# Performance work log

Measured on AMD Instinct MI355X. Metric: run time of the kernel, lower is better.

## Reference

```python
import jax, jax.numpy as jnp
import numpy as np

B, S, DIM = 1, 2048, 1024
HEADS, KV_HEADS, DH = 16, 2, 64
GQ = HEADS // KV_HEADS
CBS = 64   # compress block size
SBS = 64   # selection block size
NUM_SEL = 8
WIN = 512  # sliding window size
NUM_MEM = 1
SCALE = DH ** -0.5
NEG = -jnp.finfo(jnp.float32).max


def setup_inputs():
    ks = jax.random.split(jax.random.key(0), 12)
    cdim = CBS * DH
    dim_inner = HEADS * DH
    dim_kv = KV_HEADS * DH
    p = lambda k, shape: jax.random.normal(k, shape, jnp.float32) * 0.02
    return {
        "x": jax.random.normal(ks[0], (B, S, DIM), jnp.float32),
        "rms_g": jnp.ones((DIM,), jnp.float32),
        "W_qkv": p(ks[1], (DIM, dim_inner + 2 * dim_kv)),
        "k_pos": p(ks[2], (KV_HEADS, CBS, DH)),
        "v_pos": p(ks[3], (KV_HEADS, CBS, DH)),
        "mem_kv": p(ks[4], (2, KV_HEADS, NUM_MEM, DH)),
        "kW1": p(ks[5], (cdim, cdim)), "kb1": jnp.zeros((cdim,), jnp.float32),
        "kW2": p(ks[6], (cdim, DH)), "kb2": jnp.zeros((DH,), jnp.float32),
        "vW1": p(ks[7], (cdim, cdim)), "vb1": jnp.zeros((cdim,), jnp.float32),
        "vW2": p(ks[8], (cdim, DH)), "vb2": jnp.zeros((DH,), jnp.float32),
        "W_comb": p(ks[9], (DIM, 3 * HEADS)),
        "b_comb": jnp.tile(jnp.array([-2.0, -2.0, 2.0], jnp.float32), HEADS),
        "W_out": p(ks[10], (HEADS * DH, DIM)),
    }


def _rot_half(u):
    v = u.reshape(u.shape[:-1] + (DH // 2, 2))
    return jnp.stack([-v[..., 1], v[..., 0]], axis=-1).reshape(u.shape)


def reference(x, rms_g, W_qkv, k_pos, v_pos, mem_kv, kW1, kb1, kW2, kb2,
              vW1, vb1, vW2, vb2, W_comb, b_comb, W_out):
    n_cb = S // CBS
    n_fb = S // SBS
    num_sel = min(NUM_SEL, n_cb)

    # RMSNorm
    xn = x * jax.lax.rsqrt(jnp.mean(x * x, -1, keepdims=True) + jnp.finfo(jnp.float32).eps) * rms_g

    qkv = xn @ W_qkv
    q, k, v = jnp.split(qkv, [HEADS * DH, (HEADS + KV_HEADS) * DH], axis=-1)
    q = q.reshape(B, S, HEADS, DH).transpose(0, 2, 1, 3)       # b h n d
    k = k.reshape(B, S, KV_HEADS, DH).transpose(0, 2, 1, 3)
    v = v.reshape(B, S, KV_HEADS, DH).transpose(0, 2, 1, 3)

    # ---- compressed branch: per-block MLP compression of K/V ----
    kc = (k + jnp.tile(k_pos, (1, n_cb, 1))[None]).reshape(B, KV_HEADS, n_cb, CBS * DH)
    vc = (v + jnp.tile(v_pos, (1, n_cb, 1))[None]).reshape(B, KV_HEADS, n_cb, CBS * DH)
    ck = jax.nn.relu(kc @ kW1 + kb1) @ kW2 + kb2               # b h w d
    cv = jax.nn.relu(vc @ vW1 + vb1) @ vW2 + vb2
    ck = jnp.concatenate([jnp.broadcast_to(mem_kv[0], (B, KV_HEADS, NUM_MEM, DH)), ck], axis=2)
    cv = jnp.concatenate([jnp.broadcast_to(mem_kv[1], (B, KV_HEADS, NUM_MEM, DH)), cv], axis=2)
    ck_seq = jnp.concatenate([jnp.full((NUM_MEM,), -1), (jnp.arange(n_cb) + 1) * CBS - 1])
    cmask = ck_seq[None, :] < jnp.arange(S)[:, None]           # [S, mem+n_cb]
    qg = q.reshape(B, KV_HEADS, GQ, S, DH)
    csim = jnp.einsum('bhgid,bhjd->bhgij', qg, ck) * SCALE
    csim = jnp.where(cmask, csim, NEG)
    c_out = jnp.einsum('bhgij,bhjd->bhgid', jax.nn.softmax(csim, -1), cv).reshape(B, HEADS, S, DH)

    # ---- rotary embedding (interleaved pairs, theta=10000) ----
    inv_freq = 1.0 / (10000.0 ** (jnp.arange(0, DH, 2, dtype=jnp.float32) / DH))
    freqs = jnp.repeat(jnp.arange(S, dtype=jnp.float32)[:, None] * inv_freq, 2, axis=-1)
    cos, sin = jnp.cos(freqs), jnp.sin(freqs)
    rq = q * cos + _rot_half(q) * sin
    rk = k * cos + _rot_half(k) * sin

    # ---- block selection from compressed attention scores ----
    imp = csim[..., NUM_MEM:].mean(axis=2)                     # mean over grouped queries: [B,KVH,S,n_cb]
    imp = jnp.concatenate([jnp.full(imp.shape[:-1] + (1,), -1000.0), imp], -1)
    imp = jax.nn.softmax(imp, -1)[..., 1:]
    sel_val, sel_idx = jax.lax.top_k(imp, num_sel)             # [B,KVH,S,sel]
    fmask = jnp.broadcast_to((sel_val > 1e-10)[..., None], (B, KV_HEADS, S, num_sel, SBS))
    diag_idx = jnp.broadcast_to((jnp.arange(S) // SBS)[None, None, :, None], (B, KV_HEADS, S, 1))
    sel_idx = jnp.concatenate([sel_idx, diag_idx], -1)         # append own (diagonal) block
    causal = jnp.tril(jnp.ones((SBS, SBS), bool))
    diag_mask = jnp.broadcast_to(jnp.tile(causal, (n_fb, 1))[None, None, :, None, :], (B, KV_HEADS, S, 1, SBS))
    fmask = jnp.concatenate([fmask, diag_mask], axis=-2).reshape(B, KV_HEADS, S, (num_sel + 1) * SBS)

    # ---- fine attention over gathered selected blocks ----
    fkb = rk.reshape(B, KV_HEADS, 1, n_fb, SBS, DH)
    fvb = v.reshape(B, KV_HEADS, 1, n_fb, SBS, DH)
    gi = sel_idx[..., None, None]                              # [B,KVH,S,sel+1,1,1]
    fk = jnp.take_along_axis(fkb, gi, axis=3).reshape(B, KV_HEADS, S, (num_sel + 1) * SBS, DH)
    fv = jnp.take_along_axis(fvb, gi, axis=3).reshape(B, KV_HEADS, S, (num_sel + 1) * SBS, DH)
    fqg = rq.reshape(B, KV_HEADS, GQ, S, DH)
    fsim = jnp.einsum('bhgid,bhijd->bhgij', fqg, fk) * SCALE
    fsim = jnp.where(fmask[:, :, None], fsim, NEG)
    f_out = jnp.einsum('bhgij,bhijd->bhgid', jax.nn.softmax(fsim, -1), fv).reshape(B, HEADS, S, DH)

    # ---- causal sliding window (exact window, look_backward=1) ----
    skf = jnp.repeat(rk, GQ, axis=1)
    svf = jnp.repeat(v, GQ, axis=1)
    nw = S // WIN
    kw = skf.reshape(B, HEADS, nw, WIN, DH)
    vw = svf.reshape(B, HEADS, nw, WIN, DH)
    kcat = jnp.concatenate([jnp.pad(kw, ((0, 0), (0, 0), (1, 0), (0, 0), (0, 0)))[:, :, :nw], kw], axis=3)
    vcat = jnp.concatenate([jnp.pad(vw, ((0, 0), (0, 0), (1, 0), (0, 0), (0, 0)))[:, :, :nw], vw], axis=3)
    qw = rq.reshape(B, HEADS, nw, WIN, DH)
    gq_pos = jnp.arange(nw)[:, None, None] * WIN + jnp.arange(WIN)[None, :, None]
    gk_pos = jnp.arange(nw)[:, None, None] * WIN - WIN + jnp.arange(2 * WIN)[None, None, :]
    smask = (gk_pos >= 0) & (gk_pos <= gq_pos) & (gq_pos - gk_pos <= WIN)
    ssim = jnp.where(smask, jnp.einsum('bhwid,bhwjd->bhwij', qw, kcat) * SCALE, NEG)
    s_out = jnp.einsum('bhwij,bhwjd->bhwid', jax.nn.softmax(ssim, -1), vcat).reshape(B, HEADS, S, DH)

    # ---- learned per-token, per-head strategy combination ----
    gates = jax.nn.sigmoid(xn @ W_comb + b_comb).reshape(B, S, HEADS, 3).transpose(0, 2, 1, 3)
    out = gates[..., 0:1] * c_out + gates[..., 1:2] * f_out + gates[..., 2:3] * s_out
    return out.transpose(0, 2, 1, 3).reshape(B, S, HEADS * DH) @ W_out
```

## Files before the change

kernel.cpp:

```cpp
#include <hip/hip_runtime.h>
#include <hip/hip_bf16.h>
#include <cstddef>
#include <cstdint>

#define S      2048
#define DIM    1024
#define HEADS  16
#define KVH    2
#define GQ     8
#define DH     64
#define CBS    64
#define SBS    64
#define NUMSEL 8
#define WIN    512
#define NCB    (S / CBS)
#define CDIM   (CBS * DH)
#define QKVC   (HEADS * DH + 2 * KVH * DH)
#define KOFF   (HEADS * DH)
#define VOFF   (HEADS * DH + KVH * DH)
#define SCALE  0.125f
#define RMS_EPS 1.1920928955078125e-07f

typedef __attribute__((ext_vector_type(8))) short bf16x8;
typedef __attribute__((ext_vector_type(4))) float f32x4;

__device__ inline short f2bs(float f) {
    __hip_bfloat16 b = __float2bfloat16(f);
    return *(short*)&b;
}

__device__ inline float wave_sum(float v) {
    for (int o = 32; o > 0; o >>= 1) v += __shfl_xor(v, o);
    return v;
}

__global__ __launch_bounds__(256) void rmsnorm_kernel(
        const float* __restrict__ x, const float* __restrict__ g,
        float* __restrict__ xn, __hip_bfloat16* __restrict__ xnb) {
    int s = blockIdx.x, tid = threadIdx.x;
    const float4* row = (const float4*)(x + (size_t)s * DIM);
    float4 v = row[tid];
    float ss = v.x * v.x + v.y * v.y + v.z * v.z + v.w * v.w;
    ss = wave_sum(ss);
    __shared__ float red[4];
    if ((tid & 63) == 0) red[tid >> 6] = ss;
    __syncthreads();
    float tot = red[0] + red[1] + red[2] + red[3];
    float sc = rsqrtf(tot / (float)DIM + RMS_EPS);
    float4 gg = ((const float4*)g)[tid];
    float4 o;
    o.x = v.x * sc * gg.x; o.y = v.y * sc * gg.y;
    o.z = v.z * sc * gg.z; o.w = v.w * sc * gg.w;
    ((float4*)(xn + (size_t)s * DIM))[tid] = o;
    size_t b = (size_t)s * DIM + tid * 4;
    xnb[b + 0] = __float2bfloat16(o.x);
    xnb[b + 1] = __float2bfloat16(o.y);
    xnb[b + 2] = __float2bfloat16(o.z);
    xnb[b + 3] = __float2bfloat16(o.w);
}

__global__ __launch_bounds__(256) void cast_bf16_kernel(
        const float* __restrict__ in, __hip_bfloat16* __restrict__ out, int n4) {
    int e = blockIdx.x * 256 + threadIdx.x;
    if (e >= n4) return;
    float4 v = ((const float4*)in)[e];
    out[4 * e + 0] = __float2bfloat16(v.x);
    out[4 * e + 1] = __float2bfloat16(v.y);
    out[4 * e + 2] = __float2bfloat16(v.z);
    out[4 * e + 3] = __float2bfloat16(v.w);
}

__global__ __launch_bounds__(256) void transpose_cast_kernel(
        const float* __restrict__ W, short* __restrict__ Wt, int K, int N) {
    __shared__ float tile[64][65];
    int n0 = blockIdx.x * 64, k0 = blockIdx.y * 64;
    int tid = threadIdx.x;
    #pragma unroll
    for (int e = 0; e < 16; e++) {
        int idx = tid + e * 256;
        int r = idx >> 6, c = idx & 63;
        float v = 0.f;
        if (n0 + c < N) v = W[(size_t)(k0 + r) * N + n0 + c];
        tile[r][c] = v;
    }
    __syncthreads();
    #pragma unroll
    for (int e = 0; e < 16; e++) {
        int idx = tid + e * 256;
        int r = idx >> 6, c = idx & 63;
        if (n0 + r < N)
            Wt[(size_t)(n0 + r) * K + k0 + c] = f2bs(tile[c][r]);
    }
}

__global__ __launch_bounds__(256) void cast_v_kernel(
        const float* __restrict__ qkv, short* __restrict__ vb) {
    int e = blockIdx.x * 256 + threadIdx.x;
    if (e >= S * KVH * DH / 4) return;
    int idx = e * 4;
    int tok = idx / (KVH * DH), rem = idx % (KVH * DH);
    float4 v = *(const float4*)(qkv + (size_t)tok * QKVC + VOFF + rem);
    vb[idx + 0] = f2bs(v.x);
    vb[idx + 1] = f2bs(v.y);
    vb[idx + 2] = f2bs(v.z);
    vb[idx + 3] = f2bs(v.w);
}

template <int BM, int BN, int WM, int WN, int ACT>
__global__ __launch_bounds__(256) void gemm_bt_kernel(
        const __hip_bfloat16* __restrict__ A, const short* __restrict__ Bt,
        const float* __restrict__ bias, float* __restrict__ C,
        int M, int N, int K) {
    constexpr int BK = 32;
    constexpr int TM = BM / (WM * 16);
    constexpr int TN = BN / (WN * 16);
    constexpr int LDK = BK + 8;
    __shared__ short As[BM][LDK];
    __shared__ short Bs[BN][LDK];
    int tid = threadIdx.x;
    int wave = tid >> 6, lane = tid & 63;
    int wm = wave % WM, wn = wave / WM;
    int m0 = wm * TM * 16, n0 = wn * TN * 16;
    int bm = blockIdx.y * BM, bn = blockIdx.x * BN;
    int lm = lane & 15, quad = lane >> 4;
    const short* Ash = (const short*)A;
    f32x4 acc[TM][TN] = {};
    for (int k0 = 0; k0 < K; k0 += BK) {
        #pragma unroll
        for (int e = 0; e < BM * BK / (256 * 8); e++) {
            int idx = (tid + e * 256) * 8;
            int r = idx >> 5, kk = idx & 31;
            *(bf16x8*)(&As[r][kk]) =
                *(const bf16x8*)(Ash + (size_t)(bm + r) * K + k0 + kk);
        }
        #pragma unroll
        for (int e = 0; e < BN * BK / (256 * 8); e++) {
            int idx = (tid + e * 256) * 8;
            int r = idx >> 5, kk = idx & 31;
            bf16x8 v = {};
            if (bn + r < N)
                v = *(const bf16x8*)(Bt + (size_t)(bn + r) * K + k0 + kk);
            *(bf16x8*)(&Bs[r][kk]) = v;
        }
        __syncthreads();
        bf16x8 af[TM], bf_[TN];
        #pragma unroll
        for (int i = 0; i < TM; i++)
            af[i] = *(const bf16x8*)(&As[m0 + i * 16 + lm][quad * 8]);
        #pragma unroll
        for (int j = 0; j < TN; j++)
            bf_[j] = *(const bf16x8*)(&Bs[n0 + j * 16 + lm][quad * 8]);
        #pragma unroll
        for (int i = 0; i < TM; i++)
            #pragma unroll
            for (int j = 0; j < TN; j++)
                acc[i][j] = __builtin_amdgcn_mfma_f32_16x16x32_bf16(
                    af[i], bf_[j], acc[i][j], 0, 0, 0);
        __syncthreads();
    }
    #pragma unroll
    for (int i = 0; i < TM; i++) {
        #pragma unroll
        for (int j = 0; j < TN; j++) {
            int gn = bn + n0 + j * 16 + lm;
            if (gn >= N) continue;
            #pragma unroll
            for (int r = 0; r < 4; r++) {
                int gm = bm + m0 + i * 16 + quad * 4 + r;
                float v = acc[i][j][r];
                if (bias) v += bias[gn];
                if (ACT == 2) v = 1.f / (1.f + expf(-v));
                C[(size_t)gm * N + gn] = v;
            }
        }
    }
}

template <int BM, int BN, int WM, int WN>
__global__ __launch_bounds__(256) void gemm_mfma_kernel(
        const __hip_bfloat16* __restrict__ A, const float* __restrict__ B,
        float* __restrict__ C, int M, int N, int K, int kslice) {
    constexpr int BK = 32;
    constexpr int TM = BM / (WM * 16);
    constexpr int TN = BN / (WN * 16);
    constexpr int LDK = BK + 8;
    constexpr int NB = BN * BK / 256;
    __shared__ __hip_bfloat16 As[BM][LDK];
    __shared__ __hip_bfloat16 Bs[BN][LDK];
    int tid = threadIdx.x;
    int wave = tid >> 6, lane = tid & 63;
    int wm = wave % WM, wn = wave / WM;
    int m0 = wm * TM * 16, n0 = wn * TN * 16;
    int bm = blockIdx.y * BM, bn = blockIdx.x * BN;
    int kbeg = blockIdx.z * kslice, kend = kbeg + kslice;
    int lm = lane & 15, quad = lane >> 4;
    f32x4 acc[TM][TN] = {};
    for (int k0 = kbeg; k0 < kend; k0 += BK) {
        #pragma unroll
        for (int e = 0; e < BM * BK / (256 * 8); e++) {
            int idx = (tid + e * 256) * 8;
            int r = idx >> 5, kk = idx & 31;
            *(bf16x8*)(&As[r][kk]) =
                *(const bf16x8*)(A + (size_t)(bm + r) * K + k0 + kk);
        }
        float tmpB[NB];
        #pragma unroll
        for (int e = 0; e < NB; e++) {
            int idx = tid + e * 256;
            int kk = idx / BN, n = idx % BN;
            tmpB[e] = B[(size_t)(k0 + kk) * N + bn + n];
        }
        #pragma unroll
        for (int e = 0; e < NB; e++) {
            int idx = tid + e * 256;
            int kk = idx / BN, n = idx % BN;
            Bs[n][kk] = __float2bfloat16(tmpB[e]);
        }
        __syncthreads();
        bf16x8 af[TM], bf_[TN];
        #pragma unroll
        for (int i = 0; i < TM; i++)
            af[i] = *(const bf16x8*)(&As[m0 + i * 16 + lm][quad * 8]);
        #pragma unroll
        for (int j = 0; j < TN; j++)
            bf_[j] = *(const bf16x8*)(&Bs[n0 + j * 16 + lm][quad * 8]);
        #pragma unroll
        for (int i = 0; i < TM; i++)
            #pragma unroll
            for (int j = 0; j < TN; j++)
                acc[i][j] = __builtin_amdgcn_mfma_f32_16x16x32_bf16(
                    af[i], bf_[j], acc[i][j], 0, 0, 0);
        __syncthreads();
    }
    size_t cbase = (size_t)blockIdx.z * M * N;
    #pragma unroll
    for (int i = 0; i < TM; i++) {
        #pragma unroll
        for (int j = 0; j < TN; j++) {
            int gn = bn + n0 + j * 16 + lm;
            #pragma unroll
            for (int r = 0; r < 4; r++) {
                int gm = bm + m0 + i * 16 + quad * 4 + r;
                C[cbase + (size_t)gm * N + gn] = acc[i][j][r];
            }
        }
    }
}

__global__ __launch_bounds__(256) void gemm_splitk_kernel(
        const float* __restrict__ A, const float* __restrict__ B,
        float* __restrict__ P, int M, int N, int K, int kslice) {
    const int BM = 64, BN = 64, BK = 16;
    __shared__ float As[BK][BM + 4];
    __shared__ float Bs[BK][BN];
    int bm = blockIdx.y * BM, bn = blockIdx.x * BN;
    int z = blockIdx.z;
    int kbeg = z * kslice, kend = kbeg + kslice;
    int tid = threadIdx.x;
// ... 129 lines not shown
    }
    for (int e = t; e < NCB * DH; e += 64) {
        int w = e >> 6, d = e & 63;
        ckl[w * 65 + d] = ck[((size_t)kvh * (NCB + 1) + 1 + w) * DH + d];
    }
    __syncthreads();
    if (t < NCB) {
        int w = t;
        float val;
        if (w * CBS + CBS - 1 < s) {
            float acc = 0.f;
            #pragma unroll
            for (int g = 0; g < GQ; g++) {
                const float* qp = qg + g * DH;
                const float* cp = ckl + w * 65;
                #pragma unroll 16
                for (int d = 0; d < DH; d++) acc += qp[d] * cp[d];
            }
            val = acc * SCALE * (1.f / (float)GQ);
        } else {
            val = -INFINITY;
        }
        imp[((size_t)kvh * S + s) * NCB + w] = val;
    }
}

__global__ __launch_bounds__(256) void select_kernel(
        const float* __restrict__ imp, int* __restrict__ sel) {
    int idx = blockIdx.x * 256 + threadIdx.x;
    if (idx >= KVH * S) return;
    const float* row = imp + (size_t)idx * NCB;
    float p[NCB];
    float m = -1000.f;
    for (int w = 0; w < NCB; w++) { p[w] = row[w]; m = fmaxf(m, p[w]); }
    float z = expf(-1000.f - m);
    for (int w = 0; w < NCB; w++) { p[w] = expf(p[w] - m); z += p[w]; }
    float inv = 1.f / z;
    bool used[NCB];
    for (int w = 0; w < NCB; w++) used[w] = false;
    for (int i = 0; i < NUMSEL; i++) {
        int best = 0; float bv = -1.f;
        for (int w = 0; w < NCB; w++) {
            if (!used[w]) {
                float pw = p[w] * inv;
                if (pw > bv) { bv = pw; best = w; }
            }
        }
        used[best] = true;
        sel[(size_t)idx * NUMSEL + i] = (bv > 1e-10f) ? best : -1;
    }
}

__global__ __launch_bounds__(256) void cattn_kernel(
        const float* __restrict__ qkv, const short* __restrict__ ck16,
        const short* __restrict__ cv16, const float* __restrict__ gates,
        float* __restrict__ attn) {
    int h = blockIdx.x, qb = blockIdx.y;
    int kvh = h >> 3;
    int tid = threadIdx.x;
    int wv = tid >> 6, lane = tid & 63;
    int lm = lane & 15, quad = lane >> 4;
    __shared__ short Qb[64][72];
    __shared__ short Ks[64][72];
    __shared__ short Vt[64][72];
    __shared__ short Pb[64][72];
    for (int e = tid; e < 1024; e += 256) {
        int q = e >> 4, d4 = (e & 15) * 4;
        float4 v = *(const float4*)(qkv + (size_t)(qb * 64 + q) * QKVC + h * DH + d4);
        Qb[q][d4 + 0] = f2bs(v.x); Qb[q][d4 + 1] = f2bs(v.y);
        Qb[q][d4 + 2] = f2bs(v.z); Qb[q][d4 + 3] = f2bs(v.w);
    }
    for (int e = tid; e < 512; e += 256) {
        int c8 = e >> 6, j = e & 63;
        bf16x8 kv = {}, vv = {};
        if (j < NCB + 1) {
            kv = *(const bf16x8*)(ck16 + ((size_t)kvh * (NCB + 1) + j) * DH + c8 * 8);
            vv = *(const bf16x8*)(cv16 + ((size_t)kvh * (NCB + 1) + j) * DH + c8 * 8);
        }
        #pragma unroll
        for (int t = 0; t < 8; t++) {
            Ks[j][c8 * 8 + t] = kv[t];
            Vt[c8 * 8 + t][j] = vv[t];
        }
    }
    __syncthreads();
    bf16x8 aq0 = *(const bf16x8*)&Qb[wv * 16 + lm][quad * 8];
    bf16x8 aq1 = *(const bf16x8*)&Qb[wv * 16 + lm][32 + quad * 8];
    int vismax = (qb < NCB) ? qb : NCB;
    f32x4 sc[4];
    #pragma unroll
    for (int t = 0; t < 4; t++) {
        bf16x8 bk0 = *(const bf16x8*)&Ks[t * 16 + lm][quad * 8];
        bf16x8 bk1 = *(const bf16x8*)&Ks[t * 16 + lm][32 + quad * 8];
        f32x4 s4 = {0.f, 0.f, 0.f, 0.f};
        s4 = __builtin_amdgcn_mfma_f32_16x16x32_bf16(aq0, bk0, s4, 0, 0, 0);
        s4 = __builtin_amdgcn_mfma_f32_16x16x32_bf16(aq1, bk1, s4, 0, 0, 0);
        sc[t] = s4;
    }
    float l[4];
    float pr[4][4];
    #pragma unroll
    for (int r = 0; r < 4; r++) {
        float mx = -INFINITY;
        #pragma unroll
        for (int t = 0; t < 4; t++) {
            int jj = t * 16 + lm;
            bool vis = (jj == 0) || (jj <= vismax);
            float v = vis ? sc[t][r] * SCALE : -INFINITY;
            sc[t][r] = v;
            mx = fmaxf(mx, v);
        }
        #pragma unroll
        for (int o = 1; o < 16; o <<= 1) mx = fmaxf(mx, __shfl_xor(mx, o));
        float sum = 0.f;
        #pragma unroll
        for (int t = 0; t < 4; t++) {
            float p = __expf(sc[t][r] - mx);
            pr[r][t] = p;
            sum += p;
        }
        #pragma unroll
        for (int o = 1; o < 16; o <<= 1) sum += __shfl_xor(sum, o);
        l[r] = sum;
    }
    #pragma unroll
    for (int r = 0; r < 4; r++)
        #pragma unroll
        for (int t = 0; t < 4; t++)
            Pb[wv * 16 + quad * 4 + r][t * 16 + lm] = f2bs(pr[r][t]);
    __syncthreads();
    bf16x8 ap0 = *(const bf16x8*)&Pb[wv * 16 + lm][quad * 8];
    bf16x8 ap1 = *(const bf16x8*)&Pb[wv * 16 + lm][32 + quad * 8];
    f32x4 oacc[4];
    #pragma unroll
    for (int t = 0; t < 4; t++) {
        bf16x8 bv0 = *(const bf16x8*)&Vt[t * 16 + lm][quad * 8];
        bf16x8 bv1 = *(const bf16x8*)&Vt[t * 16 + lm][32 + quad * 8];
        f32x4 a = {0.f, 0.f, 0.f, 0.f};
        a = __builtin_amdgcn_mfma_f32_16x16x32_bf16(ap0, bv0, a, 0, 0, 0);
        a = __builtin_amdgcn_mfma_f32_16x16x32_bf16(ap1, bv1, a, 0, 0, 0);
        oacc[t] = a;
    }
    #pragma unroll
    for (int r = 0; r < 4; r++) {
        int spos = qb * 64 + wv * 16 + quad * 4 + r;
        float g0 = gates[((size_t)spos * HEADS + h) * 3 + 0];
        float f = g0 / l[r];
        #pragma unroll
        for (int t = 0; t < 4; t++)
            attn[(size_t)spos * (HEADS * DH) + h * DH + t * 16 + lm] = oacc[t][r] * f;
    }
}

__global__ __launch_bounds__(64, 2) void fattn_kernel(
        const short* __restrict__ rqb, const short* __restrict__ rkb,
        const short* __restrict__ vb, const int* __restrict__ sel,
        const float* __restrict__ gates, float* __restrict__ attn) {
    int kvh = blockIdx.x, s = blockIdx.y;
    int lane = threadIdx.x;
    int lm = lane & 15, quad = lane >> 4;
    __shared__ short Vt[64][68];
    __shared__ short Pb[16][68];
    const short* qp = rqb + (size_t)s * (HEADS * DH) + (size_t)(kvh * 8 + (lm & 7)) * DH;
    bf16x8 aq0 = *(const bf16x8*)(qp + quad * 8);
    bf16x8 aq1 = *(const bf16x8*)(qp + 32 + quad * 8);
    int bl[9];
    {
        const int4* sp = (const int4*)(sel + ((size_t)kvh * S + s) * NUMSEL);
        int4 s0 = sp[0], s1 = sp[1];
        bl[0] = s0.x; bl[1] = s0.y; bl[2] = s0.z; bl[3] = s0.w;
        bl[4] = s1.x; bl[5] = s1.y; bl[6] = s1.z; bl[7] = s1.w;
        bl[8] = s >> 6;
    }
    float m[4], l[4];
    f32x4 oacc[4];
    #pragma unroll
    for (int r = 0; r < 4; r++) {
        m[r] = -INFINITY; l[r] = 0.f;
        oacc[r] = (f32x4){0.f, 0.f, 0.f, 0.f};
    }
    bf16x8 kpre[2][4][2];
    bf16x8 vpre[2][8];
    {
        int w0 = bl[0] < 0 ? 0 : bl[0];
        #pragma unroll
        for (int t = 0; t < 4; t++) {
            const short* kp = rkb + ((size_t)(w0 * SBS + t * 16 + lm) * KVH + kvh) * DH;
            kpre[0][t][0] = *(const bf16x8*)(kp + quad * 8);
            kpre[0][t][1] = *(const bf16x8*)(kp + 32 + quad * 8);
        }
        const short* vp = vb + ((size_t)(w0 * SBS + lane) * KVH + kvh) * DH;
        #pragma unroll
        for (int r = 0; r < 8; r++) vpre[0][r] = *(const bf16x8*)(vp + r * 8);
    }
    #pragma unroll
    for (int i = 0; i < 9; i++) {
        const int p = i & 1;
        const int pn = p ^ 1;
        if (i < 8) {
            int wn = bl[i + 1] < 0 ? 0 : bl[i + 1];
            #pragma unroll
            for (int t = 0; t < 4; t++) {
                const short* kp = rkb + ((size_t)(wn * SBS + t * 16 + lm) * KVH + kvh) * DH;
                kpre[pn][t][0] = *(const bf16x8*)(kp + quad * 8);
                kpre[pn][t][1] = *(const bf16x8*)(kp + 32 + quad * 8);
            }
            const short* vp = vb + ((size_t)(wn * SBS + lane) * KVH + kvh) * DH;
            #pragma unroll
            for (int r = 0; r < 8; r++) vpre[pn][r] = *(const bf16x8*)(vp + r * 8);
        }
        if (i < 8 && bl[i] < 0) continue;
        #pragma unroll
        for (int r = 0; r < 8; r++)
            #pragma unroll
            for (int t = 0; t < 8; t++) Vt[r * 8 + t][lane] = vpre[p][r][t];
        f32x4 sc[4];
        #pragma unroll
        for (int t = 0; t < 4; t++) {
            f32x4 s4 = {0.f, 0.f, 0.f, 0.f};
            s4 = __builtin_amdgcn_mfma_f32_16x16x32_bf16(aq0, kpre[p][t][0], s4, 0, 0, 0);
            s4 = __builtin_amdgcn_mfma_f32_16x16x32_bf16(aq1, kpre[p][t][1], s4, 0, 0, 0);
            sc[t] = s4;
        }
        bool diag = (i == 8);
        #pragma unroll
        for (int r = 0; r < 4; r++) {
            float mx = -INFINITY;
            #pragma unroll
            for (int t = 0; t < 4; t++) {
                int jj = t * 16 + lm;
                bool vis = !diag || (jj <= (s & 63));
                float v = vis ? sc[t][r] * SCALE : -INFINITY;
                sc[t][r] = v;
                mx = fmaxf(mx, v);
            }
            #pragma unroll
            for (int o = 1; o < 16; o <<= 1) mx = fmaxf(mx, __shfl_xor(mx, o));
            float mn = fmaxf(m[r], mx);
            float al = __expf(m[r] - mn);
            float sum = 0.f;
            #pragma unroll
            for (int t = 0; t < 4; t++) {
                float pv_ = __expf(sc[t][r] - mn);
                sc[t][r] = pv_;
                sum += pv_;
            }
            #pragma unroll
            for (int o = 1; o < 16; o <<= 1) sum += __shfl_xor(sum, o);
            l[r] = l[r] * al + sum;
            m[r] = mn;
            #pragma unroll
            for (int t = 0; t < 4; t++) oacc[t][r] *= al;
        }
        #pragma unroll
        for (int r = 0; r < 4; r++)
            #pragma unroll
            for (int t = 0; t < 4; t++)
                Pb[quad * 4 + r][t * 16 + lm] = f2bs(sc[t][r]);
        asm volatile("s_waitcnt lgkmcnt(0)" ::: "memory");
        bf16x8 ap0 = *(const bf16x8*)&Pb[lm][quad * 8];
        bf16x8 ap1 = *(const bf16x8*)&Pb[lm][32 + quad * 8];
        #pragma unroll
        for (int t = 0; t < 4; t++) {
            bf16x8 bv0 = *(const bf16x8*)&Vt[t * 16 + lm][quad * 8];
            bf16x8 bv1 = *(const bf16x8*)&Vt[t * 16 + lm][32 + quad * 8];
            oacc[t] = __builtin_amdgcn_mfma_f32_16x16x32_bf16(ap0, bv0, oacc[t], 0, 0, 0);
            oacc[t] = __builtin_amdgcn_mfma_f32_16x16x32_bf16(ap1, bv1, oacc[t], 0, 0, 0);
        }
    }
    if (quad < 2) {
        #pragma unroll
        for (int r = 0; r < 4; r++) {
            int head = kvh * 8 + quad * 4 + r;
            float fac = gates[((size_t)s * HEADS + head) * 3 + 1] / l[r];
            #pragma unroll
            for (int t = 0; t < 4; t++)
                attn[(size_t)s * (HEADS * DH) + head * DH + t * 16 + lm]
                    += oacc[t][r] * fac;
        }
    }
}

__global__ __launch_bounds__(256) void sattn_kernel(
        const short* __restrict__ rqb, const short* __restrict__ rkb,
        const short* __restrict__ vb, const float* __restrict__ gates,
        float* __restrict__ attn) {
    int h = blockIdx.x, qb = blockIdx.y;
    int kvh = h >> 3;
    int tid = threadIdx.x;
    int wv = tid >> 6, lane = tid & 63;
    int lm = lane & 15, quad = lane >> 4;
    __shared__ short Vt[2][64][72];
    __shared__ short Pb[64][72];
    const short* qp = rqb + (size_t)(qb * 64 + wv * 16 + lm) * (HEADS * DH) + h * DH;
    bf16x8 aq0 = *(const bf16x8*)(qp + quad * 8);
    bf16x8 aq1 = *(const bf16x8*)(qp + 32 + quad * 8);
    int myrow = wv * 16 + quad * 4;
    int j0 = tid & 63, c80 = tid >> 6;
    float m[4], l[4];
    f32x4 oacc[4];
    #pragma unroll
    for (int r = 0; r < 4; r++) { m[r] = -INFINITY; l[r] = 0.f; }
    #pragma unroll
    for (int t = 0; t < 4; t++) oacc[t] = (f32x4){0.f, 0.f, 0.f, 0.f};
    int nc = 0;
    for (int c = 0; c < 9; c++) {
        int kb = qb * 64 - WIN + c * 64;
        if (kb < 0) continue;
        const short* vp = vb + ((size_t)(kb + j0) * KVH + kvh) * DH;
        bf16x8 vv0 = *(const bf16x8*)(vp + c80 * 8);
        bf16x8 vv1 = *(const bf16x8*)(vp + (c80 + 4) * 8);
        f32x4 sc[4];
        #pragma unroll
        for (int t = 0; t < 4; t++) {
            const short* kp = rkb + ((size_t)(kb + t * 16 + lm) * KVH + kvh) * DH;
            bf16x8 bk0 = *(const bf16x8*)(kp + quad * 8);
            bf16x8 bk1 = *(const bf16x8*)(kp + 32 + quad * 8);
            f32x4 s4 = {0.f, 0.f, 0.f, 0.f};
            s4 = __builtin_amdgcn_mfma_f32_16x16x32_bf16(aq0, bk0, s4, 0, 0, 0);
            s4 = __builtin_amdgcn_mfma_f32_16x16x32_bf16(aq1, bk1, s4, 0, 0, 0);
            sc[t] = s4;
        }
        short* vtb = &Vt[nc & 1][0][0];
        #pragma unroll
        for (int t = 0; t < 8; t++) vtb[(size_t)(c80 * 8 + t) * 72 + j0] = vv0[t];
        #pragma unroll
        for (int t = 0; t < 8; t++) vtb[(size_t)((c80 + 4) * 8 + t) * 72 + j0] = vv1[t];
        __syncthreads();
        #pragma unroll
        for (int r = 0; r < 4; r++) {
            int row = myrow + r;
            float mx = -INFINITY;
            #pragma unroll
            for (int t = 0; t < 4; t++) {
                int jj = t * 16 + lm;
                bool vis = true;
                if (c == 0) vis = (jj >= row);
                if (c == 8) vis = (jj <= row);
                float v = vis ? sc[t][r] * SCALE : -INFINITY;
                sc[t][r] = v;
                mx = fmaxf(mx, v);
            }
            #pragma unroll
            for (int o = 1; o < 16; o <<= 1) mx = fmaxf(mx, __shfl_xor(mx, o));
            float mn = fmaxf(m[r], mx);
            float al = __expf(m[r] - mn);
            float sum = 0.f;
            #pragma unroll
            for (int t = 0; t < 4; t++) {
                float pv_ = __expf(sc[t][r] - mn);
                sc[t][r] = pv_;
                sum += pv_;
            }
            #pragma unroll
            for (int o = 1; o < 16; o <<= 1) sum += __shfl_xor(sum, o);
            l[r] = l[r] * al + sum;
            m[r] = mn;
            #pragma unroll
            for (int t = 0; t < 4; t++) oacc[t][r] *= al;
        }
        #pragma unroll
        for (int r = 0; r < 4; r++)
            #pragma unroll
            for (int t = 0; t < 4; t++)
                Pb[myrow + r][t * 16 + lm] = f2bs(sc[t][r]);
        asm volatile("s_waitcnt lgkmcnt(0)" ::: "memory");
        bf16x8 ap0 = *(const bf16x8*)&Pb[wv * 16 + lm][quad * 8];
        bf16x8 ap1 = *(const bf16x8*)&Pb[wv * 16 + lm][32 + quad * 8];
        #pragma unroll
        for (int t = 0; t < 4; t++) {
            bf16x8 bv0 = *(const bf16x8*)(vtb + (size_t)(t * 16 + lm) * 72 + quad * 8);
            bf16x8 bv1 = *(const bf16x8*)(vtb + (size_t)(t * 16 + lm) * 72 + 32 + quad * 8);
            oacc[t] = __builtin_amdgcn_mfma_f32_16x16x32_bf16(ap0, bv0, oacc[t], 0, 0, 0);
            oacc[t] = __builtin_amdgcn_mfma_f32_16x16x32_bf16(ap1, bv1, oacc[t], 0, 0, 0);
        }
        nc++;
    }
    #pragma unroll
    for (int r = 0; r < 4; r++) {
        int spos = qb * 64 + myrow + r;
        float g2 = gates[((size_t)spos * HEADS + h) * 3 + 2];
        float f = g2 / l[r];
        #pragma unroll
        for (int t = 0; t < 4; t++)
            attn[(size_t)spos * (HEADS * DH) + h * DH + t * 16 + lm] += oacc[t][r] * f;
    }
}

extern "C" void kernel_launch(void* const* d_in, const int* in_sizes, int n_in,
                              void* d_out, int out_size, void* d_ws, size_t ws_size,
                              hipStream_t stream) {
    const float* x      = (const float*)d_in[0];
    const float* rms_g  = (const float*)d_in[1];
    const float* W_qkv  = (const float*)d_in[2];
    const float* k_pos  = (const float*)d_in[3];
    const float* v_pos  = (const float*)d_in[4];
    const float* mem_kv = (const float*)d_in[5];
    const float* kW1    = (const float*)d_in[6];
    const float* kb1    = (const float*)d_in[7];
    const float* kW2    = (const float*)d_in[8];
    const float* kb2    = (const float*)d_in[9];
    const float* vW1    = (const float*)d_in[10];
    const float* vb1    = (const float*)d_in[11];
    const float* vW2    = (const float*)d_in[12];
    const float* vb2    = (const float*)d_in[13];
    const float* W_comb = (const float*)d_in[14];
    const float* b_comb = (const float*)d_in[15];
    const float* W_out  = (const float*)d_in[16];
    float* out = (float*)d_out;

    float* ws    = (float*)d_ws;
    float* xn    = ws;
    float* qkv   = xn    + (size_t)S * DIM;
    short* rqb   = (short*)(qkv + (size_t)S * QKVC);
    short* rkb   = (short*)((float*)rqb + 1048576);
    float* R     = (float*)rkb + 131072;
    float* ck    = R     + 1048576;
    float* cv    = ck    + (size_t)KVH * (NCB + 1) * DH;
    short* ck16  = (short*)(cv + (size_t)KVH * (NCB + 1) * DH);
    short* cv16  = (short*)((float*)ck16 + 2112);
    float* imp   = (float*)cv16 + 2112;
    float* gates = imp   + (size_t)KVH * S * NCB;
    float* attn  = gates + (size_t)S * HEADS * 3;
    int*   sel   = (int*)(attn + (size_t)S * HEADS * DH);
    float* WT    = attn + (size_t)S * HEADS * DH + 8192;
    short* wqkvT = (short*)WT;
    short* woutT = (short*)(WT + 655360);
    short* wcombT= (short*)(WT + 655360 + 524288);

    __hip_bfloat16* xnb   = (__hip_bfloat16*)R;
    __hip_bfloat16* kcmb  = (__hip_bfloat16*)R;
    __hip_bfloat16* vcmb  = (__hip_bfloat16*)(R + 131072);
    float* khid  = R + 262144;
    float* vhid  = R + 524288;
    float* ckb   = R + 786432;
    float* cvb   = R + 790528;
    __hip_bfloat16* attnb = (__hip_bfloat16*)R;
    short* vbb   = (short*)imp;
    float* partW1 = attn;
    float* partW2 = imp;

    transpose_cast_kernel<<<dim3(QKVC / 64, DIM / 64), 256, 0, stream>>>(W_qkv, wqkvT, DIM, QKVC);
    transpose_cast_kernel<<<dim3(DIM / 64, DIM / 64), 256, 0, stream>>>(W_out, woutT, DIM, DIM);
    transpose_cast_kernel<<<dim3(1, DIM / 64), 256, 0, stream>>>(W_comb, wcombT, DIM, HEADS * 3);
    rmsnorm_kernel<<<S, 256, 0, stream>>>(x, rms_g, xn, xnb);
    gemm_bt_kernel<64, 64, 2, 2, 0><<<dim3(QKVC / 64, S / 64), 256, 0, stream>>>(
        xnb, wqkvT, nullptr, qkv, S, QKVC, DIM);
    gemm_bt_kernel<64, 64, 2, 2, 2><<<dim3(1, S / 64), 256, 0, stream>>>(
        xnb, wcombT, b_comb, gates, S, HEADS * 3, DIM);
    rotary_kernel<<<S, 256, 0, stream>>>(qkv, rqb, rkb);
    build_cmat_kernel<<<KVH * NCB, 256, 0, stream>>>(qkv, k_pos, v_pos, kcmb, vcmb);
    gemm_mfma_kernel<64, 128, 1, 4><<<dim3(CDIM / 128, 1, 8), 256, 0, stream>>>(
        kcmb, kW1, partW1, 64, CDIM, CDIM, CDIM / 8);
    reduce_splitk_kernel<1><<<(64 * CDIM + 255) / 256, 256, 0, stream>>>(
        partW1, kb1, khid, 64 * CDIM, CDIM, 8);
    gemm_splitk_kernel<<<dim3(1, 1, 32), 256, 0, stream>>>(khid, kW2, partW2, 64, DH, CDIM, CDIM / 32);
    reduce_splitk_kernel<0><<<(64 * DH + 255) / 256, 256, 0, stream>>>(partW2, kb2, ckb, 64 * DH, DH, 32);
    gemm_mfma_kernel<64, 128, 1, 4><<<dim3(CDIM / 128, 1, 8), 256, 0, stream>>>(
        vcmb, vW1, partW1, 64, CDIM, CDIM, CDIM / 8);
    reduce_splitk_kernel<1><<<(64 * CDIM + 255) / 256, 256, 0, stream>>>(
        partW1, vb1, vhid, 64 * CDIM, CDIM, 8);
    gemm_splitk_kernel<<<dim3(1, 1, 32), 256, 0, stream>>>(vhid, vW2, partW2, 64, DH, CDIM, CDIM / 32);
    reduce_splitk_kernel<0><<<(64 * DH + 255) / 256, 256, 0, stream>>>(partW2, vb2, cvb, 64 * DH, DH, 32);
    assemble_kernel<<<(KVH * (NCB + 1) * DH + 255) / 256, 256, 0, stream>>>(
        ckb, cvb, mem_kv, ck, cv, ck16, cv16);
    imp_kernel<<<dim3(KVH, S), 64, 0, stream>>>(qkv, ck, imp);
    select_kernel<<<(KVH * S + 255) / 256, 256, 0, stream>>>(imp, sel);
    cast_v_kernel<<<(S * KVH * DH / 4 + 255) / 256, 256, 0, stream>>>(qkv, vbb);
    cattn_kernel<<<dim3(HEADS, S / 64), 256, 0, stream>>>(qkv, ck16, cv16, gates, attn);
    fattn_kernel<<<dim3(KVH, S), 64, 0, stream>>>(rqb, rkb, vbb, sel, gates, attn);
    sattn_kernel<<<dim3(HEADS, S / 64), 256, 0, stream>>>(rqb, rkb, vbb, gates, attn);
    cast_bf16_kernel<<<(S * HEADS * DH / 4 + 255) / 256, 256, 0, stream>>>(
        attn, attnb, S * HEADS * DH / 4);
    gemm_bt_kernel<64, 64, 2, 2, 0><<<dim3(DIM / 64, S / 64), 256, 0, stream>>>(
        attnb, woutT, nullptr, out, S, DIM, DIM);
}
```

Measured before the change: 559.9 us.

## Split fine-attention selected blocks across two wavefronts with LSE merge

The fine (selected-block) attention kernel now launches two wavefronts per block. One wavefront handles selected blocks 0-3 and the other handles blocks 4-7 plus the diagonal block, each keeping its own online-softmax state. The partial results are then merged through shared memory using the max and sum statistics. This is meant to halve the serial per-block latency and raise parallelism. In exchange it drops the register double-buffered prefetch of K/V, uses more shared memory, and adds two barriers.

```diff
diff --git a/kernel.cpp b/kernel.cpp
--- a/kernel.cpp
+++ b/kernel.cpp
@@ -539,15 +539,16 @@
     }
 }
 
-__global__ __launch_bounds__(64, 2) void fattn_kernel(
+__global__ __launch_bounds__(128) void fattn_kernel(
         const short* __restrict__ rqb, const short* __restrict__ rkb,
         const short* __restrict__ vb, const int* __restrict__ sel,
         const float* __restrict__ gates, float* __restrict__ attn) {
     int kvh = blockIdx.x, s = blockIdx.y;
-    int lane = threadIdx.x;
+    int tid = threadIdx.x;
+    int wv = tid >> 6, lane = tid & 63;
     int lm = lane & 15, quad = lane >> 4;
-    __shared__ short Vt[64][68];
-    __shared__ short Pb[16][68];
+    __shared__ short Vt[2][64][68];
+    __shared__ short Pb[2][16][68];
     const short* qp = rqb + (size_t)s * (HEADS * DH) + (size_t)(kvh * 8 + (lm & 7)) * DH;
     bf16x8 aq0 = *(const bf16x8*)(qp + quad * 8);
     bf16x8 aq1 = *(const bf16x8*)(qp + 32 + quad * 8);
@@ -566,49 +567,30 @@
         m[r] = -INFINITY; l[r] = 0.f;
         oacc[r] = (f32x4){0.f, 0.f, 0.f, 0.f};
     }
-    bf16x8 kpre[2][4][2];
-    bf16x8 vpre[2][8];
-    {
-        int w0 = bl[0] < 0 ? 0 : bl[0];
+    int ibeg = wv ? 4 : 0;
+    int iend = wv ? 9 : 4;
+    for (int i = ibeg; i < iend; i++) {
+        int w = bl[i];
+        if (i < NUMSEL && w < 0) continue;
+        const short* vp = vb + ((size_t)(w * SBS + lane) * KVH + kvh) * DH;
+        bf16x8 vv[8];
+        #pragma unroll
+        for (int r = 0; r < 8; r++) vv[r] = *(const bf16x8*)(vp + r * 8);
+        f32x4 sc[4];
         #pragma unroll
         for (int t = 0; t < 4; t++) {
-            const short* kp = rkb + ((size_t)(w0 * SBS + t * 16 + lm) * KVH + kvh) * DH;
-            kpre[0][t][0] = *(const bf16x8*)(kp + quad * 8);
-            kpre[0][t][1] = *(const bf16x8*)(kp + 32 + quad * 8);
-        }
-        const short* vp = vb + ((size_t)(w0 * SBS + lane) * KVH + kvh) * DH;
-        #pragma unroll
-        for (int r = 0; r < 8; r++) vpre[0][r] = *(const bf16x8*)(vp + r * 8);
-    }
-    #pragma unroll
-    for (int i = 0; i < 9; i++) {
-        const int p = i & 1;
-        const int pn = p ^ 1;
-        if (i < 8) {
-            int wn = bl[i + 1] < 0 ? 0 : bl[i + 1];
-            #pragma unroll
-            for (int t = 0; t < 4; t++) {
-                const short* kp = rkb + ((size_t)(wn * SBS + t * 16 + lm) * KVH + kvh) * DH;
-                kpre[pn][t][0] = *(const bf16x8*)(kp + quad * 8);
-                kpre[pn][t][1] = *(const bf16x8*)(kp + 32 + quad * 8);
-            }
-            const short* vp = vb + ((size_t)(wn * SBS + lane) * KVH + kvh) * DH;
-            #pragma unroll
-            for (int r = 0; r < 8; r++) vpre[pn][r] = *(const bf16x8*)(vp + r * 8);
-        }
-        if (i < 8 && bl[i] < 0) continue;
+            const short* kp = rkb + ((size_t)(w * SBS + t * 16 + lm) * KVH + kvh) * DH;
+            bf16x8 bk0 = *(const bf16x8*)(kp + quad * 8);
+            bf16x8 bk1 = *(const bf16x8*)(kp + 32 + quad * 8);
+            f32x4 s4 = {0.f, 0.f, 0.f, 0.f};
+            s4 = __builtin_amdgcn_mfma_f32_16x16x32_bf16(aq0, bk0, s4, 0, 0, 0);
+            s4 = __builtin_amdgcn_mfma_f32_16x16x32_bf16(aq1, bk1, s4, 0, 0, 0);
+            sc[t] = s4;
+        }
         #pragma unroll
         for (int r = 0; r < 8; r++)
             #pragma unroll
-            for (int t = 0; t < 8; t++) Vt[r * 8 + t][lane] = vpre[p][r][t];
-        f32x4 sc[4];
-        #pragma unroll
-        for (int t = 0; t < 4; t++) {
-            f32x4 s4 = {0.f, 0.f, 0.f, 0.f};
-            s4 = __builtin_amdgcn_mfma_f32_16x16x32_bf16(aq0, kpre[p][t][0], s4, 0, 0, 0);
-            s4 = __builtin_amdgcn_mfma_f32_16x16x32_bf16(aq1, kpre[p][t][1], s4, 0, 0, 0);
-            sc[t] = s4;
-        }
+            for (int t = 0; t < 8; t++) Vt[wv][r * 8 + t][lane] = vv[r][t];
         bool diag = (i == 8);
         #pragma unroll
         for (int r = 0; r < 4; r++) {
@@ -643,27 +625,48 @@
         for (int r = 0; r < 4; r++)
             #pragma unroll
             for (int t = 0; t < 4; t++)
-                Pb[quad * 4 + r][t * 16 + lm] = f2bs(sc[t][r]);
+                Pb[wv][quad * 4 + r][t * 16 + lm] = f2bs(sc[t][r]);
         asm volatile("s_waitcnt lgkmcnt(0)" ::: "memory");
-        bf16x8 ap0 = *(const bf16x8*)&Pb[lm][quad * 8];
-        bf16x8 ap1 = *(const bf16x8*)&Pb[lm][32 + quad * 8];
+        bf16x8 ap0 = *(const bf16x8*)&Pb[wv][lm][quad * 8];
+        bf16x8 ap1 = *(const bf16x8*)&Pb[wv][lm][32 + quad * 8];
         #pragma unroll
         for (int t = 0; t < 4; t++) {
-            bf16x8 bv0 = *(const bf16x8*)&Vt[t * 16 + lm][quad * 8];
-            bf16x8 bv1 = *(const bf16x8*)&Vt[t * 16 + lm][32 + quad * 8];
+            bf16x8 bv0 = *(const bf16x8*)&Vt[wv][t * 16 + lm][quad * 8];
+            bf16x8 bv1 = *(const bf16x8*)&Vt[wv][t * 16 + lm][32 + quad * 8];
             oacc[t] = __builtin_amdgcn_mfma_f32_16x16x32_bf16(ap0, bv0, oacc[t], 0, 0, 0);
             oacc[t] = __builtin_amdgcn_mfma_f32_16x16x32_bf16(ap1, bv1, oacc[t], 0, 0, 0);
         }
     }
-    if (quad < 2) {
+    __syncthreads();
+    float* O1  = (float*)&Vt[1][0][0];
+    float* ML1 = (float*)&Pb[1][0][0];
+    if (wv == 1 && quad < 2) {
         #pragma unroll
         for (int r = 0; r < 4; r++) {
-            int head = kvh * 8 + quad * 4 + r;
-            float fac = gates[((size_t)s * HEADS + head) * 3 + 1] / l[r];
+            int head = quad * 4 + r;
             #pragma unroll
             for (int t = 0; t < 4; t++)
-                attn[(size_t)s * (HEADS * DH) + head * DH + t * 16 + lm]
-                    += oacc[t][r] * fac;
+                O1[head * 64 + t * 16 + lm] = oacc[t][r];
+            if (lm == 0) {
+                ML1[head * 2 + 0] = m[r];
+                ML1[head * 2 + 1] = l[r];
+            }
+        }
+    }
+    __syncthreads();
+    if (wv == 0 && quad < 2) {
+        #pragma unroll
+        for (int r = 0; r < 4; r++) {
+            int head = quad * 4 + r;
+            float m1 = ML1[head * 2 + 0], l1 = ML1[head * 2 + 1];
+            float ms = fmaxf(m[r], m1);
+            float a0 = __expf(m[r] - ms), a1 = __expf(m1 - ms);
+            float lt = l[r] * a0 + l1 * a1;
+            float fac = gates[((size_t)s * HEADS + kvh * 8 + head) * 3 + 1] / lt;
+            #pragma unroll
+            for (int t = 0; t < 4; t++)
+                attn[(size_t)s * (HEADS * DH) + (kvh * 8 + head) * DH + t * 16 + lm]
+                    += (oacc[t][r] * a0 + O1[head * 64 + t * 16 + lm] * a1) * fac;
         }
     }
 }
@@ -855,7 +858,7 @@
     select_kernel<<<(KVH * S + 255) / 256, 256, 0, stream>>>(imp, sel);
     cast_v_kernel<<<(S * KVH * DH / 4 + 255) / 256, 256, 0, stream>>>(qkv, vbb);
     cattn_kernel<<<dim3(HEADS, S / 64), 256, 0, stream>>>(qkv, ck16, cv16, gates, attn);
-    fattn_kernel<<<dim3(KVH, S), 64, 0, stream>>>(rqb, rkb, vbb, sel, gates, attn);
+    fattn_kernel<<<dim3(KVH, S), 128, 0, stream>>>(rqb, rkb, vbb, sel, gates, attn);
     sattn_kernel<<<dim3(HEADS, S / 64), 256, 0, stream>>>(rqb, rkb, vbb, gates, attn);
     cast_bf16_kernel<<<(S * HEADS * DH / 4 + 255) / 256, 256, 0, stream>>>(
         attn, attnb, S * HEADS * DH / 4);
```

Result: faster. 540.3 us (-3.5%).

## Pre-transpose V globally and drop LDS V transposes in attention kernels

Applied to the files above, without the earlier changes.

Replaces the V bf16 cast with a tiled transpose kernel that writes V as [kvh*DH+d][S], so the fine and sliding attention kernels can load MFMA B-operands for V straight from global memory. This removes the per-block LDS transposes and the barrier they needed. The fine kernel also drops its explicit register double-buffering of K/V. The sliding kernel is restructured from 256-thread blocks covering 64 queries into single-wave blocks covering 16 queries, with the window mask computed from global positions. The cost is more global traffic per query, since neighbouring single-wave blocks no longer share staged V, and less explicit prefetch overlap in the fine kernel.

```diff
diff --git a/kernel.cpp b/kernel.cpp
--- a/kernel.cpp
+++ b/kernel.cpp
@@ -93,17 +93,24 @@
     }
 }
 
-__global__ __launch_bounds__(256) void cast_v_kernel(
-        const float* __restrict__ qkv, short* __restrict__ vb) {
-    int e = blockIdx.x * 256 + threadIdx.x;
-    if (e >= S * KVH * DH / 4) return;
-    int idx = e * 4;
-    int tok = idx / (KVH * DH), rem = idx % (KVH * DH);
-    float4 v = *(const float4*)(qkv + (size_t)tok * QKVC + VOFF + rem);
-    vb[idx + 0] = f2bs(v.x);
-    vb[idx + 1] = f2bs(v.y);
-    vb[idx + 2] = f2bs(v.z);
-    vb[idx + 3] = f2bs(v.w);
+__global__ __launch_bounds__(256) void transpose_v_kernel(
+        const float* __restrict__ qkv, short* __restrict__ vtg) {
+    int k0 = blockIdx.x * 64, kvh = blockIdx.y;
+    __shared__ float tile[64][65];
+    int tid = threadIdx.x;
+    #pragma unroll
+    for (int e = 0; e < 16; e++) {
+        int idx = tid + e * 256;
+        int key = idx >> 6, d = idx & 63;
+        tile[key][d] = qkv[(size_t)(k0 + key) * QKVC + VOFF + kvh * DH + d];
+    }
+    __syncthreads();
+    #pragma unroll
+    for (int e = 0; e < 16; e++) {
+        int idx = tid + e * 256;
+        int d = idx >> 6, key = idx & 63;
+        vtg[(size_t)(kvh * DH + d) * S + k0 + key] = f2bs(tile[key][d]);
+    }
 }
 
 template <int BM, int BN, int WM, int WN, int ACT>
@@ -539,18 +546,21 @@
     }
 }
 
-__global__ __launch_bounds__(64, 2) void fattn_kernel(
+__global__ __launch_bounds__(64) void fattn_kernel(
         const short* __restrict__ rqb, const short* __restrict__ rkb,
-        const short* __restrict__ vb, const int* __restrict__ sel,
+        const short* __restrict__ vtg, const int* __restrict__ sel,
         const float* __restrict__ gates, float* __restrict__ attn) {
     int kvh = blockIdx.x, s = blockIdx.y;
     int lane = threadIdx.x;
     int lm = lane & 15, quad = lane >> 4;
-    __shared__ short Vt[64][68];
     __shared__ short Pb[16][68];
     const short* qp = rqb + (size_t)s * (HEADS * DH) + (size_t)(kvh * 8 + (lm & 7)) * DH;
     bf16x8 aq0 = *(const bf16x8*)(qp + quad * 8);
     bf16x8 aq1 = *(const bf16x8*)(qp + 32 + quad * 8);
+    const short* vrow[4];
+    #pragma unroll
+    for (int t = 0; t < 4; t++)
+        vrow[t] = vtg + (size_t)(kvh * DH + t * 16 + lm) * S;
     int bl[9];
     {
         const int4* sp = (const int4*)(sel + ((size_t)kvh * S + s) * NUMSEL);
@@ -566,47 +576,24 @@
         m[r] = -INFINITY; l[r] = 0.f;
         oacc[r] = (f32x4){0.f, 0.f, 0.f, 0.f};
     }
-    bf16x8 kpre[2][4][2];
-    bf16x8 vpre[2][8];
-    {
-        int w0 = bl[0] < 0 ? 0 : bl[0];
+    for (int i = 0; i < 9; i++) {
+        int w = bl[i];
+        if (i < NUMSEL && w < 0) continue;
+        bf16x8 bv0[4], bv1[4];
         #pragma unroll
         for (int t = 0; t < 4; t++) {
-            const short* kp = rkb + ((size_t)(w0 * SBS + t * 16 + lm) * KVH + kvh) * DH;
-            kpre[0][t][0] = *(const bf16x8*)(kp + quad * 8);
-            kpre[0][t][1] = *(const bf16x8*)(kp + 32 + quad * 8);
-        }
-        const short* vp = vb + ((size_t)(w0 * SBS + lane) * KVH + kvh) * DH;
-        #pragma unroll
-        for (int r = 0; r < 8; r++) vpre[0][r] = *(const bf16x8*)(vp + r * 8);
-    }
-    #pragma unroll
-    for (int i = 0; i < 9; i++) {
-        const int p = i & 1;
-        const int pn = p ^ 1;
-        if (i < 8) {
-            int wn = bl[i + 1] < 0 ? 0 : bl[i + 1];
-            #pragma unroll
-            for (int t = 0; t < 4; t++) {
-                const short* kp = rkb + ((size_t)(wn * SBS + t * 16 + lm) * KVH + kvh) * DH;
-                kpre[pn][t][0] = *(const bf16x8*)(kp + quad * 8);
-                kpre[pn][t][1] = *(const bf16x8*)(kp + 32 + quad * 8);
-            }
-            const short* vp = vb + ((size_t)(wn * SBS + lane) * KVH + kvh) * DH;
-            #pragma unroll
-            for (int r = 0; r < 8; r++) vpre[pn][r] = *(const bf16x8*)(vp + r * 8);
-        }
-        if (i < 8 && bl[i] < 0) continue;
-        #pragma unroll
-        for (int r = 0; r < 8; r++)
-            #pragma unroll
-            for (int t = 0; t < 8; t++) Vt[r * 8 + t][lane] = vpre[p][r][t];
+            bv0[t] = *(const bf16x8*)(vrow[t] + w * SBS + quad * 8);
+            bv1[t] = *(const bf16x8*)(vrow[t] + w * SBS + 32 + quad * 8);
+        }
         f32x4 sc[4];
         #pragma unroll
         for (int t = 0; t < 4; t++) {
+            const short* kp = rkb + ((size_t)(w * SBS + t * 16 + lm) * KVH + kvh) * DH;
+            bf16x8 bk0 = *(const bf16x8*)(kp + quad * 8);
+            bf16x8 bk1 = *(const bf16x8*)(kp + 32 + quad * 8);
             f32x4 s4 = {0.f, 0.f, 0.f, 0.f};
-            s4 = __builtin_amdgcn_mfma_f32_16x16x32_bf16(aq0, kpre[p][t][0], s4, 0, 0, 0);
-            s4 = __builtin_amdgcn_mfma_f32_16x16x32_bf16(aq1, kpre[p][t][1], s4, 0, 0, 0);
+            s4 = __builtin_amdgcn_mfma_f32_16x16x32_bf16(aq0, bk0, s4, 0, 0, 0);
+            s4 = __builtin_amdgcn_mfma_f32_16x16x32_bf16(aq1, bk1, s4, 0, 0, 0);
             sc[t] = s4;
         }
         bool diag = (i == 8);
@@ -649,10 +636,8 @@
         bf16x8 ap1 = *(const bf16x8*)&Pb[lm][32 + quad * 8];
         #pragma unroll
         for (int t = 0; t < 4; t++) {
-            bf16x8 bv0 = *(const bf16x8*)&Vt[t * 16 + lm][quad * 8];
-            bf16x8 bv1 = *(const bf16x8*)&Vt[t * 16 + lm][32 + quad * 8];
-            oacc[t] = __builtin_amdgcn_mfma_f32_16x16x32_bf16(ap0, bv0, oacc[t], 0, 0, 0);
-            oacc[t] = __builtin_amdgcn_mfma_f32_16x16x32_bf16(ap1, bv1, oacc[t], 0, 0, 0);
+            oacc[t] = __builtin_amdgcn_mfma_f32_16x16x32_bf16(ap0, bv0[t], oacc[t], 0, 0, 0);
+            oacc[t] = __builtin_amdgcn_mfma_f32_16x16x32_bf16(ap1, bv1[t], oacc[t], 0, 0, 0);
         }
     }
     if (quad < 2) {
@@ -668,35 +653,38 @@
     }
 }
 
-__global__ __launch_bounds__(256) void sattn_kernel(
+__global__ __launch_bounds__(64) void sattn_kernel(
         const short* __restrict__ rqb, const short* __restrict__ rkb,
-        const short* __restrict__ vb, const float* __restrict__ gates,
+        const short* __restrict__ vtg, const float* __restrict__ gates,
         float* __restrict__ attn) {
-    int h = blockIdx.x, qb = blockIdx.y;
+    int h = blockIdx.x, q0 = blockIdx.y * 16;
     int kvh = h >> 3;
-    int tid = threadIdx.x;
-    int wv = tid >> 6, lane = tid & 63;
+    int lane = threadIdx.x;
     int lm = lane & 15, quad = lane >> 4;
-    __shared__ short Vt[2][64][72];
-    __shared__ short Pb[64][72];
-    const short* qp = rqb + (size_t)(qb * 64 + wv * 16 + lm) * (HEADS * DH) + h * DH;
+    __shared__ short Pb[16][68];
+    const short* qp = rqb + (size_t)(q0 + lm) * (HEADS * DH) + h * DH;
     bf16x8 aq0 = *(const bf16x8*)(qp + quad * 8);
     bf16x8 aq1 = *(const bf16x8*)(qp + 32 + quad * 8);
-    int myrow = wv * 16 + quad * 4;
-    int j0 = tid & 63, c80 = tid >> 6;
+    const short* vrow[4];
+    #pragma unroll
+    for (int t = 0; t < 4; t++)
+        vrow[t] = vtg + (size_t)(kvh * DH + t * 16 + lm) * S;
+    int myrow = quad * 4;
     float m[4], l[4];
     f32x4 oacc[4];
     #pragma unroll
     for (int r = 0; r < 4; r++) { m[r] = -INFINITY; l[r] = 0.f; }
     #pragma unroll
     for (int t = 0; t < 4; t++) oacc[t] = (f32x4){0.f, 0.f, 0.f, 0.f};
-    int nc = 0;
-    for (int c = 0; c < 9; c++) {
-        int kb = qb * 64 - WIN + c * 64;
+    int kb_start = ((q0 - WIN) >> 6) << 6;
+    for (int kb = kb_start; kb <= q0 + 15; kb += 64) {
         if (kb < 0) continue;
-        const short* vp = vb + ((size_t)(kb + j0) * KVH + kvh) * DH;
-        bf16x8 vv0 = *(const bf16x8*)(vp + c80 * 8);
-        bf16x8 vv1 = *(const bf16x8*)(vp + (c80 + 4) * 8);
+        bf16x8 bv0[4], bv1[4];
+        #pragma unroll
+        for (int t = 0; t < 4; t++) {
+            bv0[t] = *(const bf16x8*)(vrow[t] + kb + quad * 8);
+            bv1[t] = *(const bf16x8*)(vrow[t] + kb + 32 + quad * 8);
+        }
         f32x4 sc[4];
         #pragma unroll
         for (int t = 0; t < 4; t++) {
@@ -708,22 +696,14 @@
             s4 = __builtin_amdgcn_mfma_f32_16x16x32_bf16(aq1, bk1, s4, 0, 0, 0);
             sc[t] = s4;
         }
-        short* vtb = &Vt[nc & 1][0][0];
-        #pragma unroll
-        for (int t = 0; t < 8; t++) vtb[(size_t)(c80 * 8 + t) * 72 + j0] = vv0[t];
-        #pragma unroll
-        for (int t = 0; t < 8; t++) vtb[(size_t)((c80 + 4) * 8 + t) * 72 + j0] = vv1[t];
-        __syncthreads();
         #pragma unroll
         for (int r = 0; r < 4; r++) {
-            int row = myrow + r;
+            int gq = q0 + myrow + r;
             float mx = -INFINITY;
             #pragma unroll
             for (int t = 0; t < 4; t++) {
-                int jj = t * 16 + lm;
-                bool vis = true;
-                if (c == 0) vis = (jj >= row);
-                if (c == 8) vis = (jj <= row);
+                int jjg = kb + t * 16 + lm;
+                bool vis = (jjg <= gq) && (gq - jjg <= WIN);
                 float v = vis ? sc[t][r] * SCALE : -INFINITY;
                 sc[t][r] = v;
                 mx = fmaxf(mx, v);
@@ -752,20 +732,17 @@
             for (int t = 0; t < 4; t++)
                 Pb[myrow + r][t * 16 + lm] = f2bs(sc[t][r]);
         asm volatile("s_waitcnt lgkmcnt(0)" ::: "memory");
-        bf16x8 ap0 = *(const bf16x8*)&Pb[wv * 16 + lm][quad * 8];
-        bf16x8 ap1 = *(const bf16x8*)&Pb[wv * 16 + lm][32 + quad * 8];
+        bf16x8 ap0 = *(const bf16x8*)&Pb[lm][quad * 8];
+        bf16x8 ap1 = *(const bf16x8*)&Pb[lm][32 + quad * 8];
         #pragma unroll
         for (int t = 0; t < 4; t++) {
-            bf16x8 bv0 = *(const bf16x8*)(vtb + (size_t)(t * 16 + lm) * 72 + quad * 8);
-            bf16x8 bv1 = *(const bf16x8*)(vtb + (size_t)(t * 16 + lm) * 72 + 32 + quad * 8);
-            oacc[t] = __builtin_amdgcn_mfma_f32_16x16x32_bf16(ap0, bv0, oacc[t], 0, 0, 0);
-            oacc[t] = __builtin_amdgcn_mfma_f32_16x16x32_bf16(ap1, bv1, oacc[t], 0, 0, 0);
-        }
-        nc++;
+            oacc[t] = __builtin_amdgcn_mfma_f32_16x16x32_bf16(ap0, bv0[t], oacc[t], 0, 0, 0);
+            oacc[t] = __builtin_amdgcn_mfma_f32_16x16x32_bf16(ap1, bv1[t], oacc[t], 0, 0, 0);
+        }
     }
     #pragma unroll
     for (int r = 0; r < 4; r++) {
-        int spos = qb * 64 + myrow + r;
+        int spos = q0 + myrow + r;
         float g2 = gates[((size_t)spos * HEADS + h) * 3 + 2];
         float f = g2 / l[r];
         #pragma unroll
@@ -823,7 +800,7 @@
     float* ckb   = R + 786432;
     float* cvb   = R + 790528;
     __hip_bfloat16* attnb = (__hip_bfloat16*)R;
-    short* vbb   = (short*)imp;
+    short* vtg   = (short*)imp;
     float* partW1 = attn;
     float* partW2 = imp;
 
@@ -853,10 +830,10 @@
         ckb, cvb, mem_kv, ck, cv, ck16, cv16);
     imp_kernel<<<dim3(KVH, S), 64, 0, stream>>>(qkv, ck, imp);
     select_kernel<<<(KVH * S + 255) / 256, 256, 0, stream>>>(imp, sel);
-    cast_v_kernel<<<(S * KVH * DH / 4 + 255) / 256, 256, 0, stream>>>(qkv, vbb);
+    transpose_v_kernel<<<dim3(S / 64, KVH), 256, 0, stream>>>(qkv, vtg);
     cattn_kernel<<<dim3(HEADS, S / 64), 256, 0, stream>>>(qkv, ck16, cv16, gates, attn);
-    fattn_kernel<<<dim3(KVH, S), 64, 0, stream>>>(rqb, rkb, vbb, sel, gates, attn);
-    sattn_kernel<<<dim3(HEADS, S / 64), 256, 0, stream>>>(rqb, rkb, vbb, gates, attn);
+    fattn_kernel<<<dim3(KVH, S), 64, 0, stream>>>(rqb, rkb, vtg, sel, gates, attn);
+    sattn_kernel<<<dim3(HEADS, S / 16), 64, 0, stream>>>(rqb, rkb, vtg, gates, attn);
     cast_bf16_kernel<<<(S * HEADS * DH / 4 + 255) / 256, 256, 0, stream>>>(
         attn, attnb, S * HEADS * DH / 4);
     gemm_bt_kernel<64, 64, 2, 2, 0><<<dim3(DIM / 64, S / 64), 256, 0, stream>>>(
```

Result: faster. 541.2 us (-3.3%).
